# Optimization experiments

Measured on AMD Instinct MI355X. Metric: run time of the kernel, lower is better.

The kernel has to match this reference:

```python
import jax, jax.numpy as jnp
import numpy as np

N, M, DIM, OUT_DIM = 50000, 512, 256, 256
NEG = -1e9


def setup_inputs() -> dict:
    key = jax.random.key(0)
    k1, k2, k3, k4, k5, k6 = jax.random.split(key, 6)
    node_features = jax.random.normal(k1, (N, DIM), dtype=jnp.float32)
    # each node assigned to one molecule (sorted segment ids)
    mol_ids = jnp.sort(jax.random.randint(k2, (N,), 0, M))
    mol_node_matrix = (mol_ids[None, :] == jnp.arange(M)[:, None]).astype(jnp.float32)  # [M, N]
    mol_node_mask = jnp.where(mol_node_matrix > 0, 0.0, NEG).astype(jnp.float32)  # [M, N]
    # Linear params (PyTorch-style uniform init)
    bound = 1.0 / np.sqrt(DIM)
    W_attend = jax.random.uniform(k3, (DIM, OUT_DIM), minval=-bound, maxval=bound, dtype=jnp.float32)
    b_attend = jax.random.uniform(k4, (OUT_DIM,), minval=-bound, maxval=bound, dtype=jnp.float32)
    w_align = jax.random.uniform(k5, (DIM, 1), minval=-bound, maxval=bound, dtype=jnp.float32)
    b_align = jax.random.uniform(k6, (1,), minval=-bound, maxval=bound, dtype=jnp.float32)
    return {"node_features": node_features, "mol_node_matrix": mol_node_matrix,
            "mol_node_mask": mol_node_mask, "W_attend": W_attend, "b_attend": b_attend,
            "w_align": w_align, "b_align": b_align}


def reference(node_features, mol_node_matrix, mol_node_mask, W_attend, b_attend, w_align, b_align):
    # h = LeakyReLU(attend(x)) : [N, out_dim]
    h = jax.nn.leaky_relu(node_features @ W_attend + b_attend, negative_slope=0.01)
    # a = align(x) : [N]  (dropout p=0 -> identity)
    a = (node_features @ w_align + b_align)[:, 0]
    # mol_node_matrix @ diag(a) == mol_node_matrix * a[None, :]  (same math, no NxN diag)
    logits = mol_node_matrix * a[None, :] + mol_node_mask  # [M, N]
    mol_node_weight = jax.nn.softmax(logits, axis=1)
    return mol_node_weight @ h, mol_node_weight
```

## Files before the change

kernel.cpp:

```cpp
#include <hip/hip_runtime.h>
#include <cstdint>
#include <cstddef>

#define N_NODES 50000
#define M_MOLS  512
#define DIMK    256
#define ODIM    256

#define NCH   99
#define CW    32
#define NSAMP (NCH * CW)
#define NGAP  (NCH - 1)

#define NB_WPACK 32
#define B2_GRID  (NGAP + NCH + 1 + NB_WPACK)

#define NF4   (N_NODES / 4)
#define HALF4 6250
#define A_CAP 1024

typedef float  f32x4  __attribute__((ext_vector_type(4)));
typedef __bf16 bf16x8 __attribute__((ext_vector_type(8)));

static __device__ __forceinline__ short f2bf(float f) {
  unsigned u = __builtin_bit_cast(unsigned, f);
  u = u + 0x7fffu + ((u >> 16) & 1u);
  return (short)(u >> 16);
}

static __device__ __forceinline__ int chunk_base(int c) {
  return (c < NCH - 1) ? c * 512 : (N_NODES - CW);
}

__global__ __launch_bounds__(256) void k_samp(
    const float* __restrict__ mat, int* __restrict__ smolid) {
  int b = blockIdx.x, t = threadIdx.x;
  int base = chunk_base(b);
  int cp = (t & 15) * 2;
  int rg = t >> 4;
  int idx = -1, idy = -1;
  const float* p0 = mat + (size_t)(rg * 32) * N_NODES + base + cp;
#pragma unroll 16
  for (int r = 0; r < 32; r++) {
    float2 v = *(const float2*)(p0 + (size_t)r * N_NODES);
    if (v.x != 0.f) idx = rg * 32 + r;
    if (v.y != 0.f) idy = rg * 32 + r;
  }
  __shared__ int sm[16][32];
  sm[rg][cp] = idx; sm[rg][cp + 1] = idy;
  __syncthreads();
  if (t < 32) {
    int best = -1;
#pragma unroll
    for (int g = 0; g < 16; g++) best = max(best, sm[g][t]);
    smolid[b * CW + t] = best;
  }
}

__global__ __launch_bounds__(256) void k_bounds(
    const float* __restrict__ mat, const float* __restrict__ W,
    const int* __restrict__ smolid, int* __restrict__ strt,
    int4* __restrict__ wp) {
  int b = blockIdx.x, t = threadIdx.x;
  if (b < NGAP) {
    int p  = chunk_base(b) + CW - 1;
    int q  = chunk_base(b + 1);
    int ag = smolid[b * CW + CW - 1];
    int bg = smolid[(b + 1) * CW];
    if (bg == ag) return;
    int Wd = q - p;
    int nr = bg - ag;
    __shared__ int f1[512];
    int wave = t >> 6, l = t & 63;
    for (int rr = wave; rr < nr; rr += 4) {
      const float* rp = mat + (size_t)(ag + 1 + rr) * N_NODES + p + 1;
      int mn = 0x7fffffff;
      for (int i = l; i < Wd; i += 64)
        if (rp[i] != 0.f) { mn = i; break; }
#pragma unroll
      for (int o = 1; o < 64; o <<= 1) mn = min(mn, __shfl_xor(mn, o));
      if (l == 0) f1[rr] = mn;
    }
    __syncthreads();
    if (t == 0) {
      int run = 0x7fffffff;
      for (int rr = nr - 1; rr >= 0; rr--) {
        run = min(run, f1[rr]);
        strt[ag + 1 + rr] = p + 1 + run;
      }
    }
  } else if (b < NGAP + NCH) {
    int cc = b - NGAP;
    if (t >= 1 && t < CW) {
      int prev = smolid[cc * CW + t - 1], cur = smolid[cc * CW + t];
      int col = chunk_base(cc) + t;
      for (int m = prev + 1; m <= cur; m++) strt[m] = col;
    }
  } else if (b == NGAP + NCH) {
    int first = smolid[0], last = smolid[NSAMP - 1];
    for (int m = t; m <= M_MOLS; m += 256) {
      if (m <= first) strt[m] = 0;
      else if (m > last) strt[m] = N_NODES;
    }
  } else {
    int g  = (b - NGAP - NCH - 1) * 256 + t;
    int l  = g & 63;
    int Ju = g >> 6;
    int J  = Ju >> 3, u = Ju & 7;
    int j  = J * 16 + (l & 15);
    int k0 = u * 32 + (l >> 4) * 8;
    short sv[8];
#pragma unroll
    for (int i = 0; i < 8; i++) sv[i] = f2bf(W[(size_t)(k0 + i) * ODIM + j]);
    wp[Ju * 64 + l] = *(int4*)sv;
  }
}

__global__ __launch_bounds__(512, 4) void k_fused(
    const float* __restrict__ x, const float* __restrict__ wa,
    const float* __restrict__ ba, const int* __restrict__ strt,
    const int4* __restrict__ wp, const float* __restrict__ bias,
    float* __restrict__ out0, float* __restrict__ out1) {
  int b = blockIdx.x;
  int m = b / 3, role = b - m * 3;
  int t = threadIdx.x;
  int seg_s = strt[m], seg_e = strt[m + 1];

  if (role != 0) {
    int s4 = seg_s >> 2, e4 = (seg_e + 3) >> 2;
    f32x4* orow = (f32x4*)out1 + (size_t)m * NF4;
    f32x4 z = {0.f, 0.f, 0.f, 0.f};
    int q0 = (role - 1) * HALF4;
    int q1 = q0 + HALF4;
    for (int q = q0 + t; q < q1; q += 512)
      if (q < s4 || q >= e4) __builtin_nontemporal_store(z, orow + q);
    return;
  }

  int L = seg_e - seg_s;
  __shared__ float a_lds[A_CAP];
  __shared__ __align__(16) short xs[16 * 256];
  __shared__ float fred[8];

  float ba0 = ba[0];
  int sub = t & 7;
  float4 wv[8];
  {
    const float4* wr = (const float4*)wa + sub * 8;
#pragma unroll
    for (int i = 0; i < 8; i++) wv[i] = wr[i];
  }
  int nit = (L + 63) >> 6;
  for (int it = 0; it < nit; it++) {
    int ro  = it * 64 + (t >> 3);
    int row = seg_s + ro;
    float s = 0.f;
    if (row < seg_e) {
      const float4* xr = (const float4*)(x + (size_t)row * DIMK) + sub * 8;
#pragma unroll
      for (int i = 0; i < 8; i++) {
        float4 xv = xr[i];
        s += xv.x * wv[i].x + xv.y * wv[i].y + xv.z * wv[i].z + xv.w * wv[i].w;
      }
    }
    s += __shfl_xor(s, 1); s += __shfl_xor(s, 2); s += __shfl_xor(s, 4);
    if (sub == 0 && row < seg_e && ro < A_CAP) a_lds[ro] = s + ba0;
  }
  __syncthreads();

  float mx = -3e38f;
  for (int i = t; i < L; i += 512) mx = fmaxf(mx, a_lds[i]);
#pragma unroll
  for (int o = 1; o < 64; o <<= 1) mx = fmaxf(mx, __shfl_xor(mx, o));
  if ((t & 63) == 0) fred[t >> 6] = mx;
  __syncthreads();
  mx = fred[0];
#pragma unroll
  for (int i = 1; i < 8; i++) mx = fmaxf(mx, fred[i]);
  __syncthreads();
  float sm = 0.f;
  for (int i = t; i < L; i += 512) sm += __expf(a_lds[i] - mx);
#pragma unroll
  for (int o = 1; o < 64; o <<= 1) sm += __shfl_xor(sm, o);
  if ((t & 63) == 0) fred[t >> 6] = sm;
  __syncthreads();
  sm = 0.f;
#pragma unroll
  for (int i = 0; i < 8; i++) sm += fred[i];
  float inv = (sm > 0.f) ? 1.f / sm : 0.f;
  for (int i = t; i < L; i += 512) a_lds[i] = __expf(a_lds[i] - mx) * inv;
  __syncthreads();

  {
    int s4 = seg_s >> 2, e4 = (seg_e + 3) >> 2;
    float4* orow = (float4*)out1 + (size_t)m * NF4;
    for (int q = s4 + t; q < e4; q += 512) {
      int n = q * 4;
      float4 o;
      o.x = (n     >= seg_s && n     < seg_e) ? a_lds[n     - seg_s] : 0.f;
      o.y = (n + 1 >= seg_s && n + 1 < seg_e) ? a_lds[n + 1 - seg_s] : 0.f;
      o.z = (n + 2 >= seg_s && n + 2 < seg_e) ? a_lds[n + 2 - seg_s] : 0.f;
      o.w = (n + 3 >= seg_s && n + 3 < seg_e) ? a_lds[n + 3 - seg_s] : 0.f;
      orow[q] = o;
    }
  }

  int wv_id = t >> 6, l = t & 63;
  bf16x8 wfrag[2][8];
#pragma unroll
  for (int t2 = 0; t2 < 2; t2++)
#pragma unroll
    for (int u = 0; u < 8; u++)
      wfrag[t2][u] = __builtin_bit_cast(bf16x8, wp[((wv_id * 2 + t2) * 8 + u) * 64 + l]);
  float bias_r[2];
#pragma unroll
  for (int t2 = 0; t2 < 2; t2++) bias_r[t2] = bias[wv_id * 32 + t2 * 16 + (l & 15)];

  float pooled[2] = {0.f, 0.f};
  int r = l & 15, g = l >> 4;
  int swr = (r & 7) << 4;

  int srow = t >> 5;
  int c0b  = (t & 31) * 16;
  int ssw  = (srow & 7) << 4;
  char* lb = (char*)xs;

  int nt2 = (L + 15) >> 4;
  for (int tile = 0; tile < nt2; tile++) {
    int base = seg_s + tile * 16;
    __syncthreads();
    {
      int n = base + srow;
      short sv[8];
      if (n < seg_e) {
        const float4* src = (const float4*)(x + (size_t)n * DIMK) + (t & 31) * 2;
        float4 A = src[0], B = src[1];
        sv[0] = f2bf(A.x); sv[1] = f2bf(A.y); sv[2] = f2bf(A.z); sv[3] = f2bf(A.w);
        sv[4] = f2bf(B.x); sv[5] = f2bf(B.y); sv[6] = f2bf(B.z); sv[7] = f2bf(B.w);
      } else {
#pragma unroll
        for (int i = 0; i < 8; i++) sv[i] = 0;
      }
      *(int4*)(lb + (srow << 9) + (c0b ^ ssw)) = *(int4*)sv;
    }
    __syncthreads();
    bf16x8 af[8];
#pragma unroll
    for (int u = 0; u < 8; u++)
      af[u] = __builtin_bit_cast(bf16x8,
                *(const int4*)(lb + (r << 9) + (((u << 6) + (g << 4)) ^ swr)));
#pragma unroll
    for (int t2 = 0; t2 < 2; t2++) {
      f32x4 acc = {0.f, 0.f, 0.f, 0.f};
#pragma unroll
      for (int u = 0; u < 8; u++)
        acc = __builtin_amdgcn_mfma_f32_16x16x32_bf16(af[u], wfrag[t2][u], acc, 0, 0, 0);
      float p = 0.f;
#pragma unroll
      for (int i = 0; i < 4; i++) {
        int ridx = tile * 16 + (g << 2) + i;
        float wgt = (ridx < L) ? a_lds[ridx] : 0.f;
        float h = acc[i] + bias_r[t2];
        h = h > 0.f ? h : 0.01f * h;
        p += wgt * h;
      }
      pooled[t2] += p;
    }
  }
#pragma unroll
  for (int t2 = 0; t2 < 2; t2++) {
    float p = pooled[t2];
    p += __shfl_xor(p, 16);
    p += __shfl_xor(p, 32);
    pooled[t2] = p;
  }
  if (l < 16) {
#pragma unroll
    for (int t2 = 0; t2 < 2; t2++)
      out0[m * ODIM + wv_id * 32 + t2 * 16 + l] = pooled[t2];
  }
}

extern "C" void kernel_launch(void* const* d_in, const int* in_sizes, int n_in,
                              void* d_out, int out_size, void* d_ws, size_t ws_size,
                              hipStream_t stream) {
  const float* x   = (const float*)d_in[0];
  const float* mat = (const float*)d_in[1];
  const float* W   = (const float*)d_in[3];
  const float* bA  = (const float*)d_in[4];
  const float* wa  = (const float*)d_in[5];
  const float* ba  = (const float*)d_in[6];

  float* out0 = (float*)d_out;
  float* out1 = out0 + (size_t)M_MOLS * ODIM;

  char* ws     = (char*)d_ws;
  int*  smolid = (int*) (ws);
  int*  strt   = (int*) (ws + 16384);
  int4* wp     = (int4*)(ws + 20480);

  k_samp  <<<NCH, 256, 0, stream>>>(mat, smolid);
  k_bounds<<<B2_GRID, 256, 0, stream>>>(mat, W, smolid, strt, wp);
  k_fused <<<M_MOLS * 3, 512, 0, stream>>>(x, wa, ba, strt, wp, bA, out0, out1);
}
```

Baseline: 56.79 us.

## Move align dot-product to a separate node-parallel stage and rebalance pooling blocks

The per-node align scores are now computed by a grid-wide pass in the bounds kernel, written to a workspace array, and no longer computed per molecule inside the fused kernel. The weight packing moves into the first kernel. The final kernel uses 256-thread pooling blocks with 4 output column tiles per wave, and four zero-fill blocks per molecule using plain stores in place of nontemporal ones. The aim is to spread the align work evenly across the machine and shorten the per-molecule critical path. The cost is an extra global write and read of the score array, and fewer waves per pooling block.

```diff
diff --git a/kernel.cpp b/kernel.cpp
--- a/kernel.cpp
+++ b/kernel.cpp
@@ -13,10 +13,17 @@
 #define NGAP  (NCH - 1)
 
 #define NB_WPACK 32
-#define B2_GRID  (NGAP + NCH + 1 + NB_WPACK)
-
+#define K0_GRID  (NCH + NB_WPACK)
+
+#define NB_ALIGN 1563
+#define K1_GRID  (NGAP + NCH + 1 + NB_ALIGN)
+
+#define POOL_BLOCKS 512
+#define WPB   4
+#define QPB   3125
+#define NB_WRITE (M_MOLS * WPB)
+#define K2_GRID  (POOL_BLOCKS + NB_WRITE)
 #define NF4   (N_NODES / 4)
-#define HALF4 6250
 #define A_CAP 1024
 
 typedef float  f32x4  __attribute__((ext_vector_type(4)));
@@ -32,35 +39,50 @@
   return (c < NCH - 1) ? c * 512 : (N_NODES - CW);
 }
 
-__global__ __launch_bounds__(256) void k_samp(
-    const float* __restrict__ mat, int* __restrict__ smolid) {
+__global__ __launch_bounds__(256) void k_prep(
+    const float* __restrict__ mat, const float* __restrict__ W,
+    int* __restrict__ smolid, int4* __restrict__ wp) {
   int b = blockIdx.x, t = threadIdx.x;
-  int base = chunk_base(b);
-  int cp = (t & 15) * 2;
-  int rg = t >> 4;
-  int idx = -1, idy = -1;
-  const float* p0 = mat + (size_t)(rg * 32) * N_NODES + base + cp;
+  if (b < NCH) {
+    int base = chunk_base(b);
+    int cp = (t & 15) * 2;
+    int rg = t >> 4;
+    int idx = -1, idy = -1;
+    const float* p0 = mat + (size_t)(rg * 32) * N_NODES + base + cp;
 #pragma unroll 16
-  for (int r = 0; r < 32; r++) {
-    float2 v = *(const float2*)(p0 + (size_t)r * N_NODES);
-    if (v.x != 0.f) idx = rg * 32 + r;
-    if (v.y != 0.f) idy = rg * 32 + r;
-  }
-  __shared__ int sm[16][32];
-  sm[rg][cp] = idx; sm[rg][cp + 1] = idy;
-  __syncthreads();
-  if (t < 32) {
-    int best = -1;
-#pragma unroll
-    for (int g = 0; g < 16; g++) best = max(best, sm[g][t]);
-    smolid[b * CW + t] = best;
-  }
-}
-
-__global__ __launch_bounds__(256) void k_bounds(
-    const float* __restrict__ mat, const float* __restrict__ W,
+    for (int r = 0; r < 32; r++) {
+      float2 v = *(const float2*)(p0 + (size_t)r * N_NODES);
+      if (v.x != 0.f) idx = rg * 32 + r;
+      if (v.y != 0.f) idy = rg * 32 + r;
+    }
+    __shared__ int sm[16][32];
+    sm[rg][cp] = idx; sm[rg][cp + 1] = idy;
+    __syncthreads();
+    if (t < 32) {
+      int best = -1;
+#pragma unroll
+      for (int g = 0; g < 16; g++) best = max(best, sm[g][t]);
+      smolid[b * CW + t] = best;
+    }
+  } else {
+    int g  = (b - NCH) * 256 + t;
+    int l  = g & 63;
+    int Ju = g >> 6;
+    int J  = Ju >> 3, u = Ju & 7;
+    int j  = J * 16 + (l & 15);
+    int k0 = u * 32 + (l >> 4) * 8;
+    short sv[8];
+#pragma unroll
+    for (int i = 0; i < 8; i++) sv[i] = f2bf(W[(size_t)(k0 + i) * ODIM + j]);
+    wp[Ju * 64 + l] = *(int4*)sv;
+  }
+}
+
+__global__ __launch_bounds__(256) void k_bal(
+    const float* __restrict__ x, const float* __restrict__ mat,
+    const float* __restrict__ wa, const float* __restrict__ ba,
     const int* __restrict__ smolid, int* __restrict__ strt,
-    int4* __restrict__ wp) {
+    float* __restrict__ a) {
   int b = blockIdx.x, t = threadIdx.x;
   if (b < NGAP) {
     int p  = chunk_base(b) + CW - 1;
@@ -103,98 +125,76 @@
       else if (m > last) strt[m] = N_NODES;
     }
   } else {
-    int g  = (b - NGAP - NCH - 1) * 256 + t;
-    int l  = g & 63;
-    int Ju = g >> 6;
-    int J  = Ju >> 3, u = Ju & 7;
-    int j  = J * 16 + (l & 15);
-    int k0 = u * 32 + (l >> 4) * 8;
-    short sv[8];
-#pragma unroll
-    for (int i = 0; i < 8; i++) sv[i] = f2bf(W[(size_t)(k0 + i) * ODIM + j]);
-    wp[Ju * 64 + l] = *(int4*)sv;
-  }
-}
-
-__global__ __launch_bounds__(512, 4) void k_fused(
-    const float* __restrict__ x, const float* __restrict__ wa,
-    const float* __restrict__ ba, const int* __restrict__ strt,
-    const int4* __restrict__ wp, const float* __restrict__ bias,
-    float* __restrict__ out0, float* __restrict__ out1) {
+    int tid = (b - NGAP - NCH - 1) * 256 + t;
+    int row = tid >> 3, sub = tid & 7;
+    if (row >= N_NODES) return;
+    const float4* xr = (const float4*)(x + (size_t)row * DIMK) + sub * 8;
+    const float4* wr = (const float4*)wa + sub * 8;
+    float s = 0.f;
+#pragma unroll
+    for (int i = 0; i < 8; i++) {
+      float4 xv = xr[i], wv = wr[i];
+      s += xv.x * wv.x + xv.y * wv.y + xv.z * wv.z + xv.w * wv.w;
+    }
+    s += __shfl_xor(s, 1); s += __shfl_xor(s, 2); s += __shfl_xor(s, 4);
+    if (sub == 0) a[row] = s + ba[0];
+  }
+}
+
+__global__ __launch_bounds__(256, 2) void k_out(
+    const float* __restrict__ x, const float* __restrict__ a,
+    const int* __restrict__ strt, const int4* __restrict__ wp,
+    const float* __restrict__ bias, float* __restrict__ out0,
+    float* __restrict__ out1) {
   int b = blockIdx.x;
-  int m = b / 3, role = b - m * 3;
   int t = threadIdx.x;
+
+  if (b >= POOL_BLOCKS) {
+    int wb = b - POOL_BLOCKS;
+    int m = wb >> 2, quarter = wb & 3;
+    int s = strt[m], e = strt[m + 1];
+    int s4 = s >> 2, e4 = (e + 3) >> 2;
+    float4* orow = (float4*)out1 + (size_t)m * NF4;
+    int q0 = quarter * QPB, q1 = q0 + QPB;
+    float4 z; z.x = z.y = z.z = z.w = 0.f;
+    for (int q = q0 + t; q < q1; q += 256)
+      if (q < s4 || q >= e4) orow[q] = z;
+    return;
+  }
+
+  int m = b;
   int seg_s = strt[m], seg_e = strt[m + 1];
-
-  if (role != 0) {
-    int s4 = seg_s >> 2, e4 = (seg_e + 3) >> 2;
-    f32x4* orow = (f32x4*)out1 + (size_t)m * NF4;
-    f32x4 z = {0.f, 0.f, 0.f, 0.f};
-    int q0 = (role - 1) * HALF4;
-    int q1 = q0 + HALF4;
-    for (int q = q0 + t; q < q1; q += 512)
-      if (q < s4 || q >= e4) __builtin_nontemporal_store(z, orow + q);
-    return;
-  }
-
   int L = seg_e - seg_s;
+
   __shared__ float a_lds[A_CAP];
   __shared__ __align__(16) short xs[16 * 256];
-  __shared__ float fred[8];
-
-  float ba0 = ba[0];
-  int sub = t & 7;
-  float4 wv[8];
-  {
-    const float4* wr = (const float4*)wa + sub * 8;
-#pragma unroll
-    for (int i = 0; i < 8; i++) wv[i] = wr[i];
-  }
-  int nit = (L + 63) >> 6;
-  for (int it = 0; it < nit; it++) {
-    int ro  = it * 64 + (t >> 3);
-    int row = seg_s + ro;
-    float s = 0.f;
-    if (row < seg_e) {
-      const float4* xr = (const float4*)(x + (size_t)row * DIMK) + sub * 8;
-#pragma unroll
-      for (int i = 0; i < 8; i++) {
-        float4 xv = xr[i];
-        s += xv.x * wv[i].x + xv.y * wv[i].y + xv.z * wv[i].z + xv.w * wv[i].w;
-      }
-    }
-    s += __shfl_xor(s, 1); s += __shfl_xor(s, 2); s += __shfl_xor(s, 4);
-    if (sub == 0 && row < seg_e && ro < A_CAP) a_lds[ro] = s + ba0;
-  }
-  __syncthreads();
-
+  __shared__ float fred[4];
+
+  for (int i = t; i < L; i += 256) a_lds[i] = a[seg_s + i];
+  __syncthreads();
   float mx = -3e38f;
-  for (int i = t; i < L; i += 512) mx = fmaxf(mx, a_lds[i]);
+  for (int i = t; i < L; i += 256) mx = fmaxf(mx, a_lds[i]);
 #pragma unroll
   for (int o = 1; o < 64; o <<= 1) mx = fmaxf(mx, __shfl_xor(mx, o));
   if ((t & 63) == 0) fred[t >> 6] = mx;
   __syncthreads();
-  mx = fred[0];
-#pragma unroll
-  for (int i = 1; i < 8; i++) mx = fmaxf(mx, fred[i]);
+  mx = fmaxf(fmaxf(fred[0], fred[1]), fmaxf(fred[2], fred[3]));
   __syncthreads();
   float sm = 0.f;
-  for (int i = t; i < L; i += 512) sm += __expf(a_lds[i] - mx);
+  for (int i = t; i < L; i += 256) sm += __expf(a_lds[i] - mx);
 #pragma unroll
   for (int o = 1; o < 64; o <<= 1) sm += __shfl_xor(sm, o);
   if ((t & 63) == 0) fred[t >> 6] = sm;
   __syncthreads();
-  sm = 0.f;
-#pragma unroll
-  for (int i = 0; i < 8; i++) sm += fred[i];
+  sm = fred[0] + fred[1] + fred[2] + fred[3];
   float inv = (sm > 0.f) ? 1.f / sm : 0.f;
-  for (int i = t; i < L; i += 512) a_lds[i] = __expf(a_lds[i] - mx) * inv;
+  for (int i = t; i < L; i += 256) a_lds[i] = __expf(a_lds[i] - mx) * inv;
   __syncthreads();
 
   {
     int s4 = seg_s >> 2, e4 = (seg_e + 3) >> 2;
     float4* orow = (float4*)out1 + (size_t)m * NF4;
-    for (int q = s4 + t; q < e4; q += 512) {
+    for (int q = s4 + t; q < e4; q += 256) {
       int n = q * 4;
       float4 o;
       o.x = (n     >= seg_s && n     < seg_e) ? a_lds[n     - seg_s] : 0.f;
@@ -205,24 +205,20 @@
     }
   }
 
-  int wv_id = t >> 6, l = t & 63;
-  bf16x8 wfrag[2][8];
-#pragma unroll
-  for (int t2 = 0; t2 < 2; t2++)
+  int wave = t >> 6, l = t & 63;
+  bf16x8 wfrag[4][8];
+#pragma unroll
+  for (int t2 = 0; t2 < 4; t2++)
 #pragma unroll
     for (int u = 0; u < 8; u++)
-      wfrag[t2][u] = __builtin_bit_cast(bf16x8, wp[((wv_id * 2 + t2) * 8 + u) * 64 + l]);
-  float bias_r[2];
-#pragma unroll
-  for (int t2 = 0; t2 < 2; t2++) bias_r[t2] = bias[wv_id * 32 + t2 * 16 + (l & 15)];
-
-  float pooled[2] = {0.f, 0.f};
+      wfrag[t2][u] = __builtin_bit_cast(bf16x8, wp[((wave * 4 + t2) * 8 + u) * 64 + l]);
+  float bias_r[4];
+#pragma unroll
+  for (int t2 = 0; t2 < 4; t2++) bias_r[t2] = bias[wave * 64 + t2 * 16 + (l & 15)];
+
+  float pooled[4] = {0.f, 0.f, 0.f, 0.f};
   int r = l & 15, g = l >> 4;
   int swr = (r & 7) << 4;
-
-  int srow = t >> 5;
-  int c0b  = (t & 31) * 16;
-  int ssw  = (srow & 7) << 4;
   char* lb = (char*)xs;
 
   int nt2 = (L + 15) >> 4;
@@ -230,18 +226,24 @@
     int base = seg_s + tile * 16;
     __syncthreads();
     {
-      int n = base + srow;
-      short sv[8];
+      int row = t >> 4;
+      int c0  = (t & 15) * 16;
+      int n   = base + row;
+      short sv[16];
       if (n < seg_e) {
-        const float4* src = (const float4*)(x + (size_t)n * DIMK) + (t & 31) * 2;
-        float4 A = src[0], B = src[1];
-        sv[0] = f2bf(A.x); sv[1] = f2bf(A.y); sv[2] = f2bf(A.z); sv[3] = f2bf(A.w);
-        sv[4] = f2bf(B.x); sv[5] = f2bf(B.y); sv[6] = f2bf(B.z); sv[7] = f2bf(B.w);
+        const float4* src = (const float4*)(x + (size_t)n * DIMK + c0);
+        float4 A = src[0], B = src[1], C = src[2], D = src[3];
+        sv[0]  = f2bf(A.x); sv[1]  = f2bf(A.y); sv[2]  = f2bf(A.z); sv[3]  = f2bf(A.w);
+        sv[4]  = f2bf(B.x); sv[5]  = f2bf(B.y); sv[6]  = f2bf(B.z); sv[7]  = f2bf(B.w);
+        sv[8]  = f2bf(C.x); sv[9]  = f2bf(C.y); sv[10] = f2bf(C.z); sv[11] = f2bf(C.w);
+        sv[12] = f2bf(D.x); sv[13] = f2bf(D.y); sv[14] = f2bf(D.z); sv[15] = f2bf(D.w);
       } else {
 #pragma unroll
-        for (int i = 0; i < 8; i++) sv[i] = 0;
+        for (int i = 0; i < 16; i++) sv[i] = 0;
       }
-      *(int4*)(lb + (srow << 9) + (c0b ^ ssw)) = *(int4*)sv;
+      int sw = (row & 7) << 4;
+      *(int4*)(lb + (row << 9) + (((c0 << 1)     ) ^ sw)) = *(int4*)(sv);
+      *(int4*)(lb + (row << 9) + (((c0 << 1) + 16) ^ sw)) = *(int4*)(sv + 8);
     }
     __syncthreads();
     bf16x8 af[8];
@@ -250,7 +252,7 @@
       af[u] = __builtin_bit_cast(bf16x8,
                 *(const int4*)(lb + (r << 9) + (((u << 6) + (g << 4)) ^ swr)));
 #pragma unroll
-    for (int t2 = 0; t2 < 2; t2++) {
+    for (int t2 = 0; t2 < 4; t2++) {
       f32x4 acc = {0.f, 0.f, 0.f, 0.f};
 #pragma unroll
       for (int u = 0; u < 8; u++)
@@ -268,7 +270,7 @@
     }
   }
 #pragma unroll
-  for (int t2 = 0; t2 < 2; t2++) {
+  for (int t2 = 0; t2 < 4; t2++) {
     float p = pooled[t2];
     p += __shfl_xor(p, 16);
     p += __shfl_xor(p, 32);
@@ -276,8 +278,8 @@
   }
   if (l < 16) {
 #pragma unroll
-    for (int t2 = 0; t2 < 2; t2++)
-      out0[m * ODIM + wv_id * 32 + t2 * 16 + l] = pooled[t2];
+    for (int t2 = 0; t2 < 4; t2++)
+      out0[m * ODIM + wave * 64 + t2 * 16 + l] = pooled[t2];
   }
 }
 
@@ -294,12 +296,13 @@
   float* out0 = (float*)d_out;
   float* out1 = out0 + (size_t)M_MOLS * ODIM;
 
-  char* ws     = (char*)d_ws;
-  int*  smolid = (int*) (ws);
-  int*  strt   = (int*) (ws + 16384);
-  int4* wp     = (int4*)(ws + 20480);
-
-  k_samp  <<<NCH, 256, 0, stream>>>(mat, smolid);
-  k_bounds<<<B2_GRID, 256, 0, stream>>>(mat, W, smolid, strt, wp);
-  k_fused <<<M_MOLS * 3, 512, 0, stream>>>(x, wa, ba, strt, wp, bA, out0, out1);
-}
+  char*  ws     = (char*)d_ws;
+  float* a      = (float*)(ws);
+  int*   smolid = (int*)  (ws + 200064);
+  int*   strt   = (int*)  (ws + 212800);
+  int4*  wp     = (int4*) (ws + 215040);
+
+  k_prep<<<K0_GRID, 256, 0, stream>>>(mat, W, smolid, wp);
+  k_bal <<<K1_GRID, 256, 0, stream>>>(x, mat, wa, ba, smolid, strt, a);
+  k_out <<<K2_GRID, 256, 0, stream>>>(x, a, strt, wp, bA, out0, out1);
+}
```

Result: faster. 52.92 us (-6.8%).

## Fold zero-fill into per-molecule block and move weight packing to first kernel

Applied to the files above, without the earlier changes.

The main kernel now launches one block per molecule instead of three, and each block zero-fills its own weight-matrix row outside the segment with regular stores rather than using two helper blocks with nontemporal stores. Weight bf16 packing moves from the boundary kernel into the first kernel. The LDS score buffer shrinks and launch bounds rise to allow more resident blocks. This removes dedicated fill blocks and their redundant segment reads, but serialises the ~100KB-per-row zero-fill with the compute in each block and risks overflow if a segment exceeds 512 nodes.

```diff
diff --git a/kernel.cpp b/kernel.cpp
--- a/kernel.cpp
+++ b/kernel.cpp
@@ -13,11 +13,11 @@
 #define NGAP  (NCH - 1)
 
 #define NB_WPACK 32
-#define B2_GRID  (NGAP + NCH + 1 + NB_WPACK)
+#define K0_GRID  (NCH + NB_WPACK)
+#define K1_GRID  (NGAP + NCH + 1)
 
 #define NF4   (N_NODES / 4)
-#define HALF4 6250
-#define A_CAP 1024
+#define A_CAP 512
 
 typedef float  f32x4  __attribute__((ext_vector_type(4)));
 typedef __bf16 bf16x8 __attribute__((ext_vector_type(8)));
@@ -32,35 +32,48 @@
   return (c < NCH - 1) ? c * 512 : (N_NODES - CW);
 }
 
-__global__ __launch_bounds__(256) void k_samp(
-    const float* __restrict__ mat, int* __restrict__ smolid) {
+__global__ __launch_bounds__(256) void k_prep(
+    const float* __restrict__ mat, const float* __restrict__ W,
+    int* __restrict__ smolid, int4* __restrict__ wp) {
   int b = blockIdx.x, t = threadIdx.x;
-  int base = chunk_base(b);
-  int cp = (t & 15) * 2;
-  int rg = t >> 4;
-  int idx = -1, idy = -1;
-  const float* p0 = mat + (size_t)(rg * 32) * N_NODES + base + cp;
+  if (b < NCH) {
+    int base = chunk_base(b);
+    int cp = (t & 15) * 2;
+    int rg = t >> 4;
+    int idx = -1, idy = -1;
+    const float* p0 = mat + (size_t)(rg * 32) * N_NODES + base + cp;
 #pragma unroll 16
-  for (int r = 0; r < 32; r++) {
-    float2 v = *(const float2*)(p0 + (size_t)r * N_NODES);
-    if (v.x != 0.f) idx = rg * 32 + r;
-    if (v.y != 0.f) idy = rg * 32 + r;
-  }
-  __shared__ int sm[16][32];
-  sm[rg][cp] = idx; sm[rg][cp + 1] = idy;
-  __syncthreads();
-  if (t < 32) {
-    int best = -1;
-#pragma unroll
-    for (int g = 0; g < 16; g++) best = max(best, sm[g][t]);
-    smolid[b * CW + t] = best;
-  }
-}
-
-__global__ __launch_bounds__(256) void k_bounds(
-    const float* __restrict__ mat, const float* __restrict__ W,
-    const int* __restrict__ smolid, int* __restrict__ strt,
-    int4* __restrict__ wp) {
+    for (int r = 0; r < 32; r++) {
+      float2 v = *(const float2*)(p0 + (size_t)r * N_NODES);
+      if (v.x != 0.f) idx = rg * 32 + r;
+      if (v.y != 0.f) idy = rg * 32 + r;
+    }
+    __shared__ int sm[16][32];
+    sm[rg][cp] = idx; sm[rg][cp + 1] = idy;
+    __syncthreads();
+    if (t < 32) {
+      int best = -1;
+#pragma unroll
+      for (int g = 0; g < 16; g++) best = max(best, sm[g][t]);
+      smolid[b * CW + t] = best;
+    }
+  } else {
+    int g  = (b - NCH) * 256 + t;
+    int l  = g & 63;
+    int Ju = g >> 6;
+    int J  = Ju >> 3, u = Ju & 7;
+    int j  = J * 16 + (l & 15);
+    int k0 = u * 32 + (l >> 4) * 8;
+    short sv[8];
+#pragma unroll
+    for (int i = 0; i < 8; i++) sv[i] = f2bf(W[(size_t)(k0 + i) * ODIM + j]);
+    wp[Ju * 64 + l] = *(int4*)sv;
+  }
+}
+
+__global__ __launch_bounds__(256) void k_bnd(
+    const float* __restrict__ mat, const int* __restrict__ smolid,
+    int* __restrict__ strt) {
   int b = blockIdx.x, t = threadIdx.x;
   if (b < NGAP) {
     int p  = chunk_base(b) + CW - 1;
@@ -96,51 +109,34 @@
       int col = chunk_base(cc) + t;
       for (int m = prev + 1; m <= cur; m++) strt[m] = col;
     }
-  } else if (b == NGAP + NCH) {
+  } else {
     int first = smolid[0], last = smolid[NSAMP - 1];
     for (int m = t; m <= M_MOLS; m += 256) {
       if (m <= first) strt[m] = 0;
       else if (m > last) strt[m] = N_NODES;
     }
-  } else {
-    int g  = (b - NGAP - NCH - 1) * 256 + t;
-    int l  = g & 63;
-    int Ju = g >> 6;
-    int J  = Ju >> 3, u = Ju & 7;
-    int j  = J * 16 + (l & 15);
-    int k0 = u * 32 + (l >> 4) * 8;
-    short sv[8];
-#pragma unroll
-    for (int i = 0; i < 8; i++) sv[i] = f2bf(W[(size_t)(k0 + i) * ODIM + j]);
-    wp[Ju * 64 + l] = *(int4*)sv;
-  }
-}
-
-__global__ __launch_bounds__(512, 4) void k_fused(
+  }
+}
+
+__global__ __launch_bounds__(512, 8) void k_main(
     const float* __restrict__ x, const float* __restrict__ wa,
     const float* __restrict__ ba, const int* __restrict__ strt,
     const int4* __restrict__ wp, const float* __restrict__ bias,
     float* __restrict__ out0, float* __restrict__ out1) {
-  int b = blockIdx.x;
-  int m = b / 3, role = b - m * 3;
+  int m = blockIdx.x;
   int t = threadIdx.x;
   int seg_s = strt[m], seg_e = strt[m + 1];
-
-  if (role != 0) {
-    int s4 = seg_s >> 2, e4 = (seg_e + 3) >> 2;
-    f32x4* orow = (f32x4*)out1 + (size_t)m * NF4;
-    f32x4 z = {0.f, 0.f, 0.f, 0.f};
-    int q0 = (role - 1) * HALF4;
-    int q1 = q0 + HALF4;
-    for (int q = q0 + t; q < q1; q += 512)
-      if (q < s4 || q >= e4) __builtin_nontemporal_store(z, orow + q);
-    return;
-  }
-
   int L = seg_e - seg_s;
+
   __shared__ float a_lds[A_CAP];
   __shared__ __align__(16) short xs[16 * 256];
   __shared__ float fred[8];
+
+  int s4 = seg_s >> 2, e4 = (seg_e + 3) >> 2;
+  float4* orow = (float4*)out1 + (size_t)m * NF4;
+  float4 z; z.x = z.y = z.z = z.w = 0.f;
+  for (int q = t; q < s4; q += 512) orow[q] = z;
+  for (int q = e4 + t; q < NF4; q += 512) orow[q] = z;
 
   float ba0 = ba[0];
   int sub = t & 7;
@@ -191,18 +187,14 @@
   for (int i = t; i < L; i += 512) a_lds[i] = __expf(a_lds[i] - mx) * inv;
   __syncthreads();
 
-  {
-    int s4 = seg_s >> 2, e4 = (seg_e + 3) >> 2;
-    float4* orow = (float4*)out1 + (size_t)m * NF4;
-    for (int q = s4 + t; q < e4; q += 512) {
-      int n = q * 4;
-      float4 o;
-      o.x = (n     >= seg_s && n     < seg_e) ? a_lds[n     - seg_s] : 0.f;
-      o.y = (n + 1 >= seg_s && n + 1 < seg_e) ? a_lds[n + 1 - seg_s] : 0.f;
-      o.z = (n + 2 >= seg_s && n + 2 < seg_e) ? a_lds[n + 2 - seg_s] : 0.f;
-      o.w = (n + 3 >= seg_s && n + 3 < seg_e) ? a_lds[n + 3 - seg_s] : 0.f;
-      orow[q] = o;
-    }
+  for (int q = s4 + t; q < e4; q += 512) {
+    int n = q * 4;
+    float4 o;
+    o.x = (n     >= seg_s && n     < seg_e) ? a_lds[n     - seg_s] : 0.f;
+    o.y = (n + 1 >= seg_s && n + 1 < seg_e) ? a_lds[n + 1 - seg_s] : 0.f;
+    o.z = (n + 2 >= seg_s && n + 2 < seg_e) ? a_lds[n + 2 - seg_s] : 0.f;
+    o.w = (n + 3 >= seg_s && n + 3 < seg_e) ? a_lds[n + 3 - seg_s] : 0.f;
+    orow[q] = o;
   }
 
   int wv_id = t >> 6, l = t & 63;
@@ -299,7 +291,7 @@
   int*  strt   = (int*) (ws + 16384);
   int4* wp     = (int4*)(ws + 20480);
 
-  k_samp  <<<NCH, 256, 0, stream>>>(mat, smolid);
-  k_bounds<<<B2_GRID, 256, 0, stream>>>(mat, W, smolid, strt, wp);
-  k_fused <<<M_MOLS * 3, 512, 0, stream>>>(x, wa, ba, strt, wp, bA, out0, out1);
-}
+  k_prep<<<K0_GRID, 256, 0, stream>>>(mat, W, smolid, wp);
+  k_bnd <<<K1_GRID, 256, 0, stream>>>(mat, smolid, strt);
+  k_main<<<M_MOLS, 512, 0, stream>>>(x, wa, ba, strt, wp, bA, out0, out1);
+}
```

After: 118.8 us. 109% more time.
